# Performance work log

Measured on AMD Instinct MI355X. Metric: run time of the kernel, lower is better.

The kernel has to match this reference:

```python
import jax, jax.numpy as jnp
import numpy as np

RADIUS = 0.1
NSAMPLE = 32


def _ball_query(radius, nsample, xyz, new_xyz):
    # xyz: (B,N,3), new_xyz: (B,npoint,3) -> idx (B,npoint,nsample) int32
    # Faithful to the CUDA ball_query: take the first nsample in-radius indices
    # (in ascending point order); pad with the first found index.
    N = xyz.shape[1]
    d2 = jnp.sum((new_xyz[:, :, None, :] - xyz[:, None, :, :]) ** 2, axis=-1)  # (B,np,N)
    mask = d2 < radius * radius
    key_arr = jnp.where(mask, jnp.arange(N, dtype=jnp.int32), jnp.int32(N))
    idx = jnp.sort(key_arr, axis=-1)[..., :nsample]  # (B,np,ns)
    first = idx[..., :1]
    idx = jnp.where(idx == N, first, idx)
    idx = jnp.where(idx == N, 0, idx)  # empty-ball fallback (matches zero-init buffer)
    return idx


def _group(features, idx):
    # features (B,C,N), idx (B,np,ns) -> (B,C,np,ns)
    return jax.vmap(lambda f, i: f[:, i])(features, idx)


def _forward(xyz, new_xyz):
    idx = jax.lax.stop_gradient(_ball_query(RADIUS, NSAMPLE, xyz, new_xyz))
    xyz_t = jnp.transpose(xyz, (0, 2, 1))                 # (B,3,N)
    g = _group(xyz_t, idx)                                # (B,3,np,ns) grouped_xyz
    c = jnp.transpose(new_xyz, (0, 2, 1))[..., None]      # (B,3,np,1)  new_xyz_reshaped

    # pairwise distances within each group
    diff = g[..., :, None] - g[..., None, :]              # (B,3,np,ns,ns)
    dis = jnp.sqrt(jnp.sum(diff * diff, axis=1))          # (B,np,ns,ns)
    mean_dis = jnp.mean(dis, axis=3)                      # (B,np,ns)
    tip_idx = jnp.argmax(mean_dis, axis=2)                # (B,np)
    tip_pts = jnp.take_along_axis(g, tip_idx[:, None, :, None], axis=3)[..., 0]  # (B,3,np)

    cb = jnp.broadcast_to(c, g.shape)                     # (B,3,np,ns)
    gpv = jnp.cross(jnp.cross(cb, g, axis=1), cb, axis=1)
    gpv = gpv / jnp.linalg.norm(gpv, axis=1)[:, None]     # (B,3,np,ns)

    new_r = jnp.sqrt(jnp.sum(c * c, axis=1))              # (B,np,1)
    new_norm = c / (new_r[:, None] + 1e-8)                # (B,3,np,1)

    c3 = c[..., 0]                                        # (B,3,np)
    tpv = jnp.cross(jnp.cross(c3, tip_pts, axis=1), c3, axis=1)
    tpv = tpv / jnp.linalg.norm(tpv, axis=1)[:, None]     # (B,3,np)

    gcv = jnp.cross(gpv, jnp.broadcast_to(tpv[..., None], gpv.shape), axis=1)
    sinv = jnp.sum(gcv * new_norm, axis=1)                # (B,np,ns)

    dis_t = jnp.transpose(dis, (0, 2, 1, 3))              # (B,ns,np,ns)
    dis_sort = jnp.sort(dis_t, axis=1) * sinv[:, None]    # (B,ns,np,ns)
    grouped_r = jnp.sqrt(jnp.sum(g * g, axis=1))          # (B,np,ns)
    return jnp.concatenate([dis_sort, grouped_r[:, None]], axis=1)  # (B,ns+1,np,ns)


def setup_inputs() -> dict:
    key = jax.random.key(0)
    k1, k2 = jax.random.split(key)
    xyz = jax.random.uniform(k1, (4, 16384, 3), dtype=jnp.float32)
    new_xyz = jax.random.uniform(k2, (4, 2048, 3), dtype=jnp.float32)
    return {"xyz": xyz, "new_xyz": new_xyz}


def reference(xyz, new_xyz):
    return _forward(xyz, new_xyz)
```

## Files before the change

kernel.cpp:

```cpp
#include <hip/hip_runtime.h>


#define BB 4
#define NN 16384
#define MM 2048
#define NS 32
#define R2 0.01f
#define GZ 20
#define NCELL 2000
#define CPAD 2048
#define HCAP 128

#define WS_CUR_OFF (32 * 1024)
#define WS_CNT_OFF (64 * 1024)
#define WS_PTS_OFF (96 * 1024)
#define WS_NEED (WS_PTS_OFF + (size_t)BB * NN * 16)

__device__ __forceinline__ int cell_of(float x, float y, float z) {
    int ci = (int)(x * 10.0f); ci = ci < 0 ? 0 : (ci > 9 ? 9 : ci);
    int cj = (int)(y * 10.0f); cj = cj < 0 ? 0 : (cj > 9 ? 9 : cj);
    int ck = (int)(z * 20.0f); ck = ck < 0 ? 0 : (ck > 19 ? 19 : ck);
    return (ci * 10 + cj) * GZ + ck;
}

__global__ __launch_bounds__(256) void k_count(const float* __restrict__ xyz,
                                               int* __restrict__ cnt) {
    int i = blockIdx.x * 256 + threadIdx.x;
    int b = i >> 14;
    const float* p = xyz + (size_t)i * 3;
    atomicAdd(&cnt[b * CPAD + cell_of(p[0], p[1], p[2])], 1);
}

__global__ __launch_bounds__(1024) void k_scan(const int* __restrict__ cnt,
                                               int* __restrict__ off,
                                               int* __restrict__ cur) {
    __shared__ int wsum[16];
    const int b = blockIdx.x, t = threadIdx.x;
    const int lane = t & 63, wid = t >> 6;
    int v0 = cnt[b * CPAD + 2 * t];
    int v1 = cnt[b * CPAD + 2 * t + 1];
    int s = v0 + v1;
    int x = s;
    #pragma unroll
    for (int o = 1; o < 64; o <<= 1) {
        int u = __shfl_up(x, o);
        if (lane >= o) x += u;
    }
    if (lane == 63) wsum[wid] = x;
    __syncthreads();
    int pre = 0;
    #pragma unroll
    for (int i2 = 0; i2 < 16; ++i2) pre += (i2 < wid) ? wsum[i2] : 0;
    int incl = x + pre;
    int excl = incl - s;
    off[b * CPAD + 2 * t] = excl;
    off[b * CPAD + 2 * t + 1] = excl + v0;
    cur[b * CPAD + 2 * t] = excl;
    cur[b * CPAD + 2 * t + 1] = excl + v0;
}

__global__ __launch_bounds__(256) void k_scatter(const float* __restrict__ xyz,
                                                 int* __restrict__ cur,
                                                 float4* __restrict__ pts) {
    int i = blockIdx.x * 256 + threadIdx.x;
    int b = i >> 14;
    const float* p = xyz + (size_t)i * 3;
    float x = p[0], y = p[1], z = p[2];
    int pos = atomicAdd(&cur[b * CPAD + cell_of(x, y, z)], 1);
    pts[(size_t)b * NN + pos] = make_float4(x, y, z, __int_as_float(i & (NN - 1)));
}

__global__ __launch_bounds__(256) void qgr_grid_kernel(
    const float* __restrict__ xyz,
    const float* __restrict__ nxyz,
    const int* __restrict__ offi,
    const float4* __restrict__ pts,
    float* __restrict__ out) {

    __shared__ float4 s_hit[4][2][HCAP];
    __shared__ float4 s_sel[4][2][NS];

    const int lane = threadIdx.x & 63;
    const int w = threadIdx.x >> 6;
    const int sub = lane & 31;
    const int half = lane >> 5;
    const int q0 = blockIdx.x * 8 + w * 2;
    const int b = q0 >> 11;

    const float* xb = xyz + (size_t)b * NN * 3;
    const float* nq = nxyz + (size_t)q0 * 3;
    const float cx0 = nq[0], cy0 = nq[1], cz0 = nq[2];
    const float cx1 = nq[3], cy1 = nq[4], cz1 = nq[5];
    const unsigned long long lmask = (1ull << lane) - 1ull;

    const int* offb = offi + b * CPAD;
    const float4* ptsb = pts + (size_t)b * NN;

    int hits01[2];
    for (int tq = 0; tq < 2; ++tq) {
        const float ccx = tq ? cx1 : cx0;
        const float ccy = tq ? cy1 : cy0;
        const float ccz = tq ? cz1 : cz0;

        int ci0 = (int)(ccx * 10.0f); ci0 = ci0 < 0 ? 0 : (ci0 > 9 ? 9 : ci0);
        int cj0 = (int)(ccy * 10.0f); cj0 = cj0 < 0 ? 0 : (cj0 > 9 ? 9 : cj0);
        int ck0 = (int)(ccz * 20.0f); ck0 = ck0 < 0 ? 0 : (ck0 > 19 ? 19 : ck0);
        int zlo = ck0 > 2 ? ck0 - 2 : 0;
        int zhi = ck0 < 17 ? ck0 + 2 : 19;

        int rs[9], rl[9];
        #pragma unroll
        for (int r = 0; r < 9; ++r) { rs[r] = 0; rl[r] = 0; }
        int nr = 0;
        #pragma unroll
        for (int di = -1; di <= 1; ++di) {
            int ii = ci0 + di; if ((unsigned)ii > 9u) continue;
            #pragma unroll
            for (int dj = -1; dj <= 1; ++dj) {
                int jj = cj0 + dj; if ((unsigned)jj > 9u) continue;
                int base2 = (ii * 10 + jj) * GZ;
                int s0 = offb[base2 + zlo];
                int e0 = offb[base2 + zhi + 1];
                int len = e0 - s0;
                if (len > 0) { rs[nr] = s0; rl[nr] = len; ++nr; }
            }
        }

        float4 P[9];
        #pragma unroll
        for (int r = 0; r < 9; ++r) {
            int a = (lane < rl[r]) ? (rs[r] + lane) : 0;
            P[r] = ptsb[a];
        }

        int hits = 0;
        #pragma unroll
        for (int r = 0; r < 9; ++r) {
            float dx = __fsub_rn(ccx, P[r].x);
            float dy = __fsub_rn(ccy, P[r].y);
            float dz = __fsub_rn(ccz, P[r].z);
            float d2 = __fadd_rn(__fadd_rn(__fmul_rn(dx, dx), __fmul_rn(dy, dy)),
                                 __fmul_rn(dz, dz));
            bool hit = (lane < rl[r]) && (d2 < R2);
            unsigned long long bal = __ballot(hit);
            if (bal) {
                int rank = __popcll(bal & lmask);
                int slot = hits + rank;
                if (hit && slot < HCAP) s_hit[w][tq][slot] = P[r];
                hits += __popcll(bal);
            }
        }
        for (int r = 0; r < nr; ++r) {
            for (int t0 = 64; t0 < rl[r]; t0 += 64) {
                int t = t0 + lane;
                bool act = t < rl[r];
                float4 Q = ptsb[rs[r] + (act ? t : 0)];
                float dx = __fsub_rn(ccx, Q.x);
                float dy = __fsub_rn(ccy, Q.y);
                float dz = __fsub_rn(ccz, Q.z);
                float d2 = __fadd_rn(__fadd_rn(__fmul_rn(dx, dx), __fmul_rn(dy, dy)),
                                     __fmul_rn(dz, dz));
                bool hit = act && (d2 < R2);
                unsigned long long bal = __ballot(hit);
                if (bal) {
                    int rank = __popcll(bal & lmask);
                    int slot = hits + rank;
                    if (hit && slot < HCAP) s_hit[w][tq][slot] = Q;
                    hits += __popcll(bal);
                }
            }
        }
        hits01[tq] = hits;
    }

    const int hits = half ? hits01[1] : hits01[0];
    const int cap = hits < HCAP ? hits : HCAP;
    const float ccx = half ? cx1 : cx0;
    const float ccy = half ? cy1 : cy0;
    const float ccz = half ? cz1 : cz0;

    int key[4];
    #pragma unroll
    for (int r = 0; r < 4; ++r) {
        int e = r * 32 + sub;
        int idx_e = __float_as_int(s_hit[w][half][e].w);
        key[r] = (e < cap) ? ((idx_e << 8) | e) : 0x7fffffff;
    }

    #pragma unroll
    for (int k = 2; k <= 16; k <<= 1) {
        #pragma unroll
        for (int j = k >> 1; j > 0; j >>= 1) {
            bool lower = (sub & j) == 0;
            bool asc = (sub & k) == 0;
            bool keepmin = (lower == asc);
            #pragma unroll
            for (int r = 0; r < 4; ++r) {
                int p = __shfl_xor(key[r], j);
                key[r] = keepmin ? min(key[r], p) : max(key[r], p);
            }
        }
    }
    #pragma unroll
    for (int j = 16; j > 0; j >>= 1) {
        bool lower = (sub & j) == 0;
        #pragma unroll
        for (int r = 0; r < 4; ++r) {
            int p = __shfl_xor(key[r], j);
            bool asc = (r & 1) == 0;
            key[r] = (lower == asc) ? min(key[r], p) : max(key[r], p);
        }
    }
    {
        int t0 = min(key[0], key[1]); key[1] = max(key[0], key[1]); key[0] = t0;
        int t2 = max(key[2], key[3]); key[3] = min(key[2], key[3]); key[2] = t2;
    }
    #pragma unroll
    for (int j = 16; j > 0; j >>= 1) {
        bool lower = (sub & j) == 0;
        #pragma unroll
        for (int r = 0; r < 4; ++r) {
            int p = __shfl_xor(key[r], j);
            bool asc = (r & 2) == 0;
            key[r] = (lower == asc) ? min(key[r], p) : max(key[r], p);
        }
    }
    {
        int t0 = min(key[0], key[2]); key[2] = max(key[0], key[2]); key[0] = t0;
        int t1 = min(key[1], key[3]); key[3] = max(key[1], key[3]); key[1] = t1;
        t0 = min(key[0], key[1]); key[1] = max(key[0], key[1]); key[0] = t0;
        t1 = min(key[2], key[3]); key[3] = max(key[2], key[3]); key[2] = t1;
    }
    #pragma unroll
    for (int j = 16; j > 0; j >>= 1) {
        bool lower = (sub & j) == 0;
        #pragma unroll
        for (int r = 0; r < 4; ++r) {
            int p = __shfl_xor(key[r], j);
            key[r] = lower ? min(key[r], p) : max(key[r], p);
        }
    }

    const int found = hits < NS ? hits : NS;
    const int hbase = half << 5;
    float4 sel = make_float4(0.f, 0.f, 0.f, 0.f);
    if (sub < found) sel = s_hit[w][half][key[0] & 0xFF];
    float p0x, p0y, p0z;
    if (found == 0) { p0x = xb[0]; p0y = xb[1]; p0z = xb[2]; }
    else {
        p0x = __shfl(sel.x, hbase); p0y = __shfl(sel.y, hbase); p0z = __shfl(sel.z, hbase);
    }
    if (sub >= found) { sel.x = p0x; sel.y = p0y; sel.z = p0z; }
    const float hx = sel.x, hy = sel.y, hz = sel.z;

    s_sel[w][half][sub] = sel;

    float v[NS];
    #pragma unroll
    for (int ii = 0; ii < NS; ++ii) {
        float4 B = s_sel[w][half][ii];
        float dx = __fsub_rn(B.x, hx);
        float dy = __fsub_rn(B.y, hy);
        float dz = __fsub_rn(B.z, hz);
        v[ii] = sqrtf(__fadd_rn(__fadd_rn(__fmul_rn(dx, dx), __fmul_rn(dy, dy)),
                                __fmul_rn(dz, dz)));
    }

    float r8[8];
    #pragma unroll
    for (int t = 0; t < 8; ++t) {
        r8[t] = __fadd_rn(__fadd_rn(__fadd_rn(v[t], v[t + 8]), v[t + 16]), v[t + 24]);
    }
    float mv = __fadd_rn(__fadd_rn(__fadd_rn(r8[0], r8[1]), __fadd_rn(r8[2], r8[3])),
                         __fadd_rn(__fadd_rn(r8[4], r8[5]), __fadd_rn(r8[6], r8[7])));
    int mi = sub;
    #pragma unroll
    for (int off = 1; off < 32; off <<= 1) {
        float ov = __shfl_xor(mv, off);
        int oi = __shfl_xor(mi, off);
        if (ov > mv || (ov == mv && oi < mi)) { mv = ov; mi = oi; }
    }

    float4 T = s_sel[w][half][mi];
    const float tx = T.x, ty = T.y, tz = T.z;

    float ux = ccy * tz - ccz * ty, uy = ccz * tx - ccx * tz, uz = ccx * ty - ccy * tx;
    float vx = uy * ccz - uz * ccy, vy = uz * ccx - ux * ccz, vz = ux * ccy - uy * ccx;
    float vn = fmaxf(sqrtf(vx * vx + vy * vy + vz * vz), 1e-37f);
    float tnx = vx / vn, tny = vy / vn, tnz = vz / vn;

    float nrm = sqrtf(ccx * ccx + ccy * ccy + ccz * ccz);
    float dn = nrm + 1e-8f;
    float nnx = ccx / dn, nny = ccy / dn, nnz = ccz / dn;

    float ax = ccy * hz - ccz * hy, ay = ccz * hx - ccx * hz, az = ccx * hy - ccy * hx;
    float px = ay * ccz - az * ccy, py = az * ccx - ax * ccz, pz = ax * ccy - ay * ccx;
    float pn = fmaxf(sqrtf(px * px + py * py + pz * pz), 1e-37f);
    px /= pn; py /= pn; pz /= pn;

    float qx = py * tnz - pz * tny;
    float qy = pz * tnx - px * tnz;
    float qz = px * tny - py * tnx;
    float sinv = qx * nnx + qy * nny + qz * nnz;

    float gr = sqrtf(hx * hx + hy * hy + hz * hz);

    const int m_h = (q0 + half) & (MM - 1);
    const size_t rowstride = (size_t)MM * NS;
    const size_t obase = (((size_t)b * 33) * MM + m_h) * NS + sub;
    out[obase + 32 * rowstride] = gr;

    #pragma unroll
    for (int p = 1; p < NS; p <<= 1) {
        #pragma unroll
        for (int k = p; k >= 1; k >>= 1) {
            #pragma unroll
            for (int j = k & (p - 1); j + k < NS; j += 2 * k) {
                #pragma unroll
                for (int i = 0; i < k; ++i) {
                    if (i + j + k < NS) {
                        int x = i + j, y = i + j + k;
                        if ((x / (2 * p)) == (y / (2 * p))) {
                            float lo = fminf(v[x], v[y]);
                            v[y] = fmaxf(v[x], v[y]);
                            v[x] = lo;
                        }
                    }
                }
            }
        }
    }

    #pragma unroll
    for (int ii = 0; ii < NS; ++ii)
        out[obase + (size_t)ii * rowstride] = v[ii] * sinv;
}

#define CHUNKS 4
__global__ __launch_bounds__(256) void qgr_kernel(
    const float* __restrict__ xyz,
    const float* __restrict__ nxyz,
    float* __restrict__ out) {

    __shared__ float s_gx[4][NS], s_gy[4][NS], s_gz[4][NS];
    __shared__ float s_dis[4][NS][NS + 1];

    const int lane = threadIdx.x & 63;
    const int w = threadIdx.x >> 6;
    const int q = blockIdx.x * 4 + w;
    const int b = q >> 11;
    const int m = q & (MM - 1);

    const float* xb = xyz + (size_t)b * NN * 3;
    const float* nq = nxyz + (size_t)q * 3;
    const float cx = nq[0], cy = nq[1], cz = nq[2];
    const unsigned long long lmask = (1ull << lane) - 1ull;

    int cnt = 0;
    for (int base = 0; base < NN; base += 64 * CHUNKS) {
        float X[CHUNKS], Y[CHUNKS], Z[CHUNKS];
        #pragma unroll
        for (int c = 0; c < CHUNKS; ++c) {
            const float* p = xb + (size_t)(base + c * 64 + lane) * 3;
            X[c] = p[0]; Y[c] = p[1]; Z[c] = p[2];
        }
        bool in[CHUNKS];
        #pragma unroll
        for (int c = 0; c < CHUNKS; ++c) {
            float dx = __fsub_rn(cx, X[c]);
            float dy = __fsub_rn(cy, Y[c]);
            float dz = __fsub_rn(cz, Z[c]);
            float d2 = __fadd_rn(__fadd_rn(__fmul_rn(dx, dx), __fmul_rn(dy, dy)),
                                 __fmul_rn(dz, dz));
            in[c] = d2 < R2;
        }
        #pragma unroll
        for (int c = 0; c < CHUNKS; ++c) {
            unsigned long long bal = __ballot(in[c]);
            if (bal) {
                int rank = __popcll(bal & lmask);
                int slot = cnt + rank;
                if (in[c] && slot < NS) {
                    s_gx[w][slot] = X[c]; s_gy[w][slot] = Y[c]; s_gz[w][slot] = Z[c];
                }
                cnt += __popcll(bal);
            }
        }
        if (cnt >= NS) break;
    }
    __syncthreads();

    int found = cnt < NS ? cnt : NS;
    float p0x, p0y, p0z;
    if (found == 0) { p0x = xb[0]; p0y = xb[1]; p0z = xb[2]; }
    else            { p0x = s_gx[w][0]; p0y = s_gy[w][0]; p0z = s_gz[w][0]; }
    if (lane < NS && lane >= found) {
        s_gx[w][lane] = p0x; s_gy[w][lane] = p0y; s_gz[w][lane] = p0z;
    }
    __syncthreads();

    #pragma unroll
    for (int t = 0; t < 16; ++t) {
        int e = t * 64 + lane;
        int di = e >> 5, dj = e & 31;
        float dx = __fsub_rn(s_gx[w][di], s_gx[w][dj]);
        float dy = __fsub_rn(s_gy[w][di], s_gy[w][dj]);
        float dz = __fsub_rn(s_gz[w][di], s_gz[w][dj]);
        s_dis[w][di][dj] =
            sqrtf(__fadd_rn(__fadd_rn(__fmul_rn(dx, dx), __fmul_rn(dy, dy)), __fmul_rn(dz, dz)));
    }
    __syncthreads();

    {
        int i = lane & 31;
        float r[8];
        #pragma unroll
        for (int t = 0; t < 8; ++t) {
            r[t] = __fadd_rn(__fadd_rn(__fadd_rn(s_dis[w][i][t], s_dis[w][i][t + 8]),
                                        s_dis[w][i][t + 16]),
                             s_dis[w][i][t + 24]);
        }
        float mv = __fadd_rn(__fadd_rn(__fadd_rn(r[0], r[1]), __fadd_rn(r[2], r[3])),
                             __fadd_rn(__fadd_rn(r[4], r[5]), __fadd_rn(r[6], r[7])));
        int mi = i;
        #pragma unroll
        for (int off = 1; off < 64; off <<= 1) {
            float ov = __shfl_xor(mv, off);
            int oi = __shfl_xor(mi, off);
            if (ov > mv || (ov == mv && oi < mi)) { mv = ov; mi = oi; }
        }
        float tx = s_gx[w][mi], ty = s_gy[w][mi], tz = s_gz[w][mi];
        float ux = cy * tz - cz * ty, uy = cz * tx - cx * tz, uz = cx * ty - cy * tx;
        float vx = uy * cz - uz * cy, vy = uz * cx - ux * cz, vz = ux * cy - uy * cx;
        float vn = fmaxf(sqrtf(vx * vx + vy * vy + vz * vz), 1e-37f);
        float tnx = vx / vn, tny = vy / vn, tnz = vz / vn;
        float nr = sqrtf(cx * cx + cy * cy + cz * cz);
        float dn = nr + 1e-8f;
        float nnx = cx / dn, nny = cy / dn, nnz = cz / dn;
        int j = lane & 31;
        float gx = s_gx[w][j], gy = s_gy[w][j], gz = s_gz[w][j];
        float ax = cy * gz - cz * gy, ay = cz * gx - cx * gz, az = cx * gy - cy * gx;
        float px = ay * cz - az * cy, py = az * cx - ax * cz, pz = ax * cy - ay * cx;
        float pn = fmaxf(sqrtf(px * px + py * py + pz * pz), 1e-37f);
        px /= pn; py /= pn; pz /= pn;
        float qx = py * tnz - pz * tny;
        float qy = pz * tnx - px * tnz;
        float qz = px * tny - py * tnx;
        float sinv = qx * nnx + qy * nny + qz * nnz;
        float gr = sqrtf(gx * gx + gy * gy + gz * gz);
        const size_t rowstride = (size_t)MM * NS;
        const size_t obase = (((size_t)b * 33) * MM + m) * NS + j;
        if (lane < NS) out[obase + 32 * rowstride] = gr;
        float v[NS];
        #pragma unroll
        for (int ii = 0; ii < NS; ++ii) v[ii] = s_dis[w][ii][j];
        #pragma unroll
        for (int k = 2; k <= NS; k <<= 1) {
            #pragma unroll
            for (int jj = k >> 1; jj > 0; jj >>= 1) {
                #pragma unroll
                for (int ii = 0; ii < NS; ++ii) {
                    int ll = ii ^ jj;
                    if (ll > ii) {
                        bool up = ((ii & k) == 0);
                        float a = v[ii], c2 = v[ll];
                        bool sw = up ? (a > c2) : (a < c2);
                        if (sw) { v[ii] = c2; v[ll] = a; }
                    }
                }
            }
        }
        if (lane < NS) {
            #pragma unroll
            for (int ii = 0; ii < NS; ++ii)
                out[obase + (size_t)ii * rowstride] = v[ii] * sinv;
        }
    }
}

extern "C" void kernel_launch(void* const* d_in, const int* in_sizes, int n_in,
                              void* d_out, int out_size, void* d_ws, size_t ws_size,
                              hipStream_t stream) {
    (void)in_sizes; (void)n_in; (void)out_size;
    const float* xyz = (const float*)d_in[0];
    const float* nxyz = (const float*)d_in[1];
    float* out = (float*)d_out;

    if (d_ws != nullptr && ws_size >= WS_NEED) {
        char* ws = (char*)d_ws;
        int* off = (int*)ws;
        int* cur = (int*)(ws + WS_CUR_OFF);
        int* cnt = (int*)(ws + WS_CNT_OFF);
        float4* pts = (float4*)(ws + WS_PTS_OFF);

        hipMemsetAsync(cnt, 0, 32 * 1024, stream);
        k_count<<<(BB * NN) / 256, 256, 0, stream>>>(xyz, cnt);
        k_scan<<<BB, 1024, 0, stream>>>(cnt, off, cur);
        k_scatter<<<(BB * NN) / 256, 256, 0, stream>>>(xyz, cur, pts);
        qgr_grid_kernel<<<(BB * MM) / 8, 256, 0, stream>>>(xyz, nxyz, off, pts, out);
    } else {
        qgr_kernel<<<(BB * MM) / 4, 256, 0, stream>>>(xyz, nxyz, out);
    }
}
```

Measured before the change: 98.76 us.

## Prune grid columns by exact XY distance and batch point loads for both queries

For each neighbouring xy grid column, the query now computes the minimum xy distance to the column and skips it when that already exceeds the radius. It also narrows the z-cell range to the remaining vertical extent, so fewer candidate points are scanned. The first-wave point loads for both queries in a wave are now issued together before any distance tests, to overlap memory latency. The scan kernel is reshaped to 256 threads with 8 cells each. The trade-offs are higher register pressure from the doubled arrays and a small epsilon margin on the pruning bounds.

```diff
diff --git a/kernel.cpp b/kernel.cpp
--- a/kernel.cpp
+++ b/kernel.cpp
@@ -31,15 +31,16 @@
     atomicAdd(&cnt[b * CPAD + cell_of(p[0], p[1], p[2])], 1);
 }
 
-__global__ __launch_bounds__(1024) void k_scan(const int* __restrict__ cnt,
-                                               int* __restrict__ off,
-                                               int* __restrict__ cur) {
-    __shared__ int wsum[16];
+__global__ __launch_bounds__(256) void k_scan(const int* __restrict__ cnt,
+                                              int* __restrict__ off,
+                                              int* __restrict__ cur) {
+    __shared__ int wsum[4];
     const int b = blockIdx.x, t = threadIdx.x;
-    const int lane = t & 63, wid = t >> 6;
-    int v0 = cnt[b * CPAD + 2 * t];
-    int v1 = cnt[b * CPAD + 2 * t + 1];
-    int s = v0 + v1;
+    int base = b * CPAD + t * 8;
+    int c[8]; int s = 0;
+    #pragma unroll
+    for (int k = 0; k < 8; ++k) { c[k] = cnt[base + k]; s += c[k]; }
+    int lane = t & 63, wid = t >> 6;
     int x = s;
     #pragma unroll
     for (int o = 1; o < 64; o <<= 1) {
@@ -50,13 +51,12 @@
     __syncthreads();
     int pre = 0;
     #pragma unroll
-    for (int i2 = 0; i2 < 16; ++i2) pre += (i2 < wid) ? wsum[i2] : 0;
-    int incl = x + pre;
-    int excl = incl - s;
-    off[b * CPAD + 2 * t] = excl;
-    off[b * CPAD + 2 * t + 1] = excl + v0;
-    cur[b * CPAD + 2 * t] = excl;
-    cur[b * CPAD + 2 * t + 1] = excl + v0;
+    for (int i2 = 0; i2 < 4; ++i2) pre += (i2 < wid) ? wsum[i2] : 0;
+    int excl = x + pre - s;
+    #pragma unroll
+    for (int k = 0; k < 8; ++k) {
+        off[base + k] = excl; cur[base + k] = excl; excl += c[k];
+    }
 }
 
 __global__ __launch_bounds__(256) void k_scatter(const float* __restrict__ xyz,
@@ -96,65 +96,80 @@
     const int* offb = offi + b * CPAD;
     const float4* ptsb = pts + (size_t)b * NN;
 
-    int hits01[2];
+    int rs[2][9], rl[2][9], nr[2];
+    #pragma unroll
     for (int tq = 0; tq < 2; ++tq) {
         const float ccx = tq ? cx1 : cx0;
         const float ccy = tq ? cy1 : cy0;
         const float ccz = tq ? cz1 : cz0;
-
         int ci0 = (int)(ccx * 10.0f); ci0 = ci0 < 0 ? 0 : (ci0 > 9 ? 9 : ci0);
         int cj0 = (int)(ccy * 10.0f); cj0 = cj0 < 0 ? 0 : (cj0 > 9 ? 9 : cj0);
-        int ck0 = (int)(ccz * 20.0f); ck0 = ck0 < 0 ? 0 : (ck0 > 19 ? 19 : ck0);
-        int zlo = ck0 > 2 ? ck0 - 2 : 0;
-        int zhi = ck0 < 17 ? ck0 + 2 : 19;
-
-        int rs[9], rl[9];
-        #pragma unroll
-        for (int r = 0; r < 9; ++r) { rs[r] = 0; rl[r] = 0; }
-        int nr = 0;
+        #pragma unroll
+        for (int r = 0; r < 9; ++r) { rs[tq][r] = 0; rl[tq][r] = 0; }
+        int n = 0;
         #pragma unroll
         for (int di = -1; di <= 1; ++di) {
             int ii = ci0 + di; if ((unsigned)ii > 9u) continue;
+            float xlo = ii * 0.1f, xhi = xlo + 0.1f;
+            float dxm = fmaxf(0.f, fmaxf(xlo - ccx, ccx - xhi));
             #pragma unroll
             for (int dj = -1; dj <= 1; ++dj) {
                 int jj = cj0 + dj; if ((unsigned)jj > 9u) continue;
+                float ylo = jj * 0.1f, yhi = ylo + 0.1f;
+                float dym = fmaxf(0.f, fmaxf(ylo - ccy, ccy - yhi));
+                float dxy2 = dxm * dxm + dym * dym;
+                if (dxy2 >= R2 + 1e-6f) continue;
+                float zh = sqrtf(fmaxf(R2 - dxy2, 0.f)) + 1e-3f;
+                int zlo = (int)((ccz - zh) * 20.f); if (zlo < 0) zlo = 0;
+                int zhi = (int)((ccz + zh) * 20.f); if (zhi > 19) zhi = 19;
                 int base2 = (ii * 10 + jj) * GZ;
                 int s0 = offb[base2 + zlo];
                 int e0 = offb[base2 + zhi + 1];
                 int len = e0 - s0;
-                if (len > 0) { rs[nr] = s0; rl[nr] = len; ++nr; }
-            }
-        }
-
-        float4 P[9];
+                if (len > 0) { rs[tq][n] = s0; rl[tq][n] = len; ++n; }
+            }
+        }
+        nr[tq] = n;
+    }
+
+    float4 P[2][9];
+    #pragma unroll
+    for (int tq = 0; tq < 2; ++tq) {
         #pragma unroll
         for (int r = 0; r < 9; ++r) {
-            int a = (lane < rl[r]) ? (rs[r] + lane) : 0;
-            P[r] = ptsb[a];
-        }
-
+            int a = (lane < rl[tq][r]) ? (rs[tq][r] + lane) : 0;
+            P[tq][r] = ptsb[a];
+        }
+    }
+
+    int hits01[2];
+    #pragma unroll
+    for (int tq = 0; tq < 2; ++tq) {
+        const float ccx = tq ? cx1 : cx0;
+        const float ccy = tq ? cy1 : cy0;
+        const float ccz = tq ? cz1 : cz0;
         int hits = 0;
         #pragma unroll
         for (int r = 0; r < 9; ++r) {
-            float dx = __fsub_rn(ccx, P[r].x);
-            float dy = __fsub_rn(ccy, P[r].y);
-            float dz = __fsub_rn(ccz, P[r].z);
+            float dx = __fsub_rn(ccx, P[tq][r].x);
+            float dy = __fsub_rn(ccy, P[tq][r].y);
+            float dz = __fsub_rn(ccz, P[tq][r].z);
             float d2 = __fadd_rn(__fadd_rn(__fmul_rn(dx, dx), __fmul_rn(dy, dy)),
                                  __fmul_rn(dz, dz));
-            bool hit = (lane < rl[r]) && (d2 < R2);
+            bool hit = (lane < rl[tq][r]) && (d2 < R2);
             unsigned long long bal = __ballot(hit);
             if (bal) {
                 int rank = __popcll(bal & lmask);
                 int slot = hits + rank;
-                if (hit && slot < HCAP) s_hit[w][tq][slot] = P[r];
+                if (hit && slot < HCAP) s_hit[w][tq][slot] = P[tq][r];
                 hits += __popcll(bal);
             }
         }
-        for (int r = 0; r < nr; ++r) {
-            for (int t0 = 64; t0 < rl[r]; t0 += 64) {
+        for (int r = 0; r < nr[tq]; ++r) {
+            for (int t0 = 64; t0 < rl[tq][r]; t0 += 64) {
                 int t = t0 + lane;
-                bool act = t < rl[r];
-                float4 Q = ptsb[rs[r] + (act ? t : 0)];
+                bool act = t < rl[tq][r];
+                float4 Q = ptsb[rs[tq][r] + (act ? t : 0)];
                 float dx = __fsub_rn(ccx, Q.x);
                 float dy = __fsub_rn(ccy, Q.y);
                 float dz = __fsub_rn(ccz, Q.z);
@@ -186,7 +201,6 @@
         int idx_e = __float_as_int(s_hit[w][half][e].w);
         key[r] = (e < cap) ? ((idx_e << 8) | e) : 0x7fffffff;
     }
-
     #pragma unroll
     for (int k = 2; k <= 16; k <<= 1) {
         #pragma unroll
@@ -495,7 +509,7 @@
 
         hipMemsetAsync(cnt, 0, 32 * 1024, stream);
         k_count<<<(BB * NN) / 256, 256, 0, stream>>>(xyz, cnt);
-        k_scan<<<BB, 1024, 0, stream>>>(cnt, off, cur);
+        k_scan<<<BB, 256, 0, stream>>>(cnt, off, cur);
         k_scatter<<<(BB * NN) / 256, 256, 0, stream>>>(xyz, cur, pts);
         qgr_grid_kernel<<<(BB * MM) / 8, 256, 0, stream>>>(xyz, nxyz, off, pts, out);
     } else {
```

After: 115.1 us. 1.17x slower.
